# Performance work log

Hardware: AMD Instinct MI355X
Metric: run time of the kernel (lower is better)

Reference implementation:

```python
import jax, jax.numpy as jnp
import numpy as np

Z_DIM = 256
N_MOD = 8
CAT = Z_DIM * N_MOD          # 2048
YS = 1024
B = 4096
EPS = 1e-5


def _layer_norm(x, g, b):
    mu = jnp.mean(x, axis=-1, keepdims=True)
    var = jnp.mean((x - mu) ** 2, axis=-1, keepdims=True)
    return (x - mu) * jax.lax.rsqrt(var + EPS) * g + b


def setup_inputs() -> dict:
    key = jax.random.key(0)
    ks = jax.random.split(key, 16)
    s_cat = 1.0 / np.sqrt(CAT)
    s_ys = 1.0 / np.sqrt(YS)
    return {
        "z_stack": jax.random.normal(ks[0], (N_MOD, B, Z_DIM), jnp.float32),
        "Wq": jax.random.normal(ks[1], (CAT, CAT), jnp.float32) * s_cat,
        "bq": jnp.zeros((CAT,), jnp.float32),
        "Wk": jax.random.normal(ks[2], (CAT, CAT), jnp.float32) * s_cat,
        "bk": jnp.zeros((CAT,), jnp.float32),
        "Wv": jax.random.normal(ks[3], (CAT, CAT), jnp.float32) * s_cat,
        "bv": jnp.zeros((CAT,), jnp.float32),
        "W1": jax.random.normal(ks[4], (CAT, YS), jnp.float32) * s_cat,
        "b1": jnp.zeros((YS,), jnp.float32),
        "W2": jax.random.normal(ks[5], (YS, CAT), jnp.float32) * s_ys,
        "b2": jnp.zeros((CAT,), jnp.float32),
        "ln1_g": jnp.ones((CAT,), jnp.float32),
        "ln1_b": jnp.zeros((CAT,), jnp.float32),
        "ln2_g": jnp.ones((CAT,), jnp.float32),
        "ln2_b": jnp.zeros((CAT,), jnp.float32),
        "Wys": jax.random.normal(ks[6], (CAT, YS), jnp.float32) * s_cat,
        "bys": jnp.zeros((YS,), jnp.float32),
        "Ws": jax.random.normal(ks[7], (N_MOD, YS, Z_DIM), jnp.float32) * s_ys,
        "bs": jnp.zeros((N_MOD, Z_DIM), jnp.float32),
    }


def reference(z_stack, Wq, bq, Wk, bk, Wv, bv, W1, b1, W2, b2,
              ln1_g, ln1_b, ln2_g, ln2_b, Wys, bys, Ws, bs):
    M, Bn, Zd = z_stack.shape
    # torch.cat(z, dim=1): [B, M*Zd]
    x = jnp.transpose(z_stack, (1, 0, 2)).reshape(Bn, M * Zd)
    # self-attention over the batch dim (unscaled, as in source)
    q = x @ Wq + bq
    k = x @ Wk + bk
    v = x @ Wv + bv
    attended = jax.nn.softmax(q @ k.T, axis=-1) @ v  # [B, B] scores
    # dropout is identity in eval mode
    x = _layer_norm(x + attended, ln1_g, ln1_b)
    h = jax.nn.gelu(x @ W1 + b1, approximate=False) @ W2 + b2
    h = _layer_norm(x + h, ln2_g, ln2_b)
    yb = h @ Wys + bys                               # [B, YS]
    # per-module scaling layers, stacked output [M, B, Zd]
    y = jnp.einsum('bs,msz->mbz', yb, Ws) + bs[:, None, :]
    return y
```

## Files before the change

### kernel.cpp

```cpp
#include <hip/hip_runtime.h>
#include <hip/hip_bf16.h>
#include <cstdint>
#include <cstddef>
#include <math.h>

typedef __bf16 bf16x8 __attribute__((ext_vector_type(8)));
typedef float  f32x4  __attribute__((ext_vector_type(4)));

#define DEVI __device__ __forceinline__

static constexpr int BB = 4096;
static constexpr int ZD = 256;

DEVI unsigned short f2bf(float f) {
  __bf16 h = (__bf16)f;
  return __builtin_bit_cast(unsigned short, h);
}
DEVI float bf2f(unsigned short u) {
  return (float)__builtin_bit_cast(__bf16, u);
}

DEVI void gload_lds16(const void* g, void* l) {
  __builtin_amdgcn_global_load_lds(
      (__attribute__((address_space(1))) void*)(g),
      (__attribute__((address_space(3))) void*)(l), 16, 0, 0);
}

DEVI int swz(int L) { return L ^ (((L >> 7) & 7) << 4); }

__global__ __launch_bounds__(256) void pack_x(
    const float* __restrict__ z, unsigned short* __restrict__ x2) {
  const int i = (blockIdx.x * 256 + threadIdx.x) * 4;
  const int m  = i >> 20;
  const int r  = i & 1048575;
  const int b  = r >> 8;
  const int zd = r & 255;
  const float4 v = *(const float4*)(z + i);
  ushort4 h, l;
  h.x = f2bf(v.x); l.x = f2bf(v.x - bf2f(h.x));
  h.y = f2bf(v.y); l.y = f2bf(v.y - bf2f(h.y));
  h.z = f2bf(v.z); l.z = f2bf(v.z - bf2f(h.z));
  h.w = f2bf(v.w); l.w = f2bf(v.w - bf2f(h.w));
  const size_t o2 = (size_t)b * 4096 + m * ZD + zd;
  *(ushort4*)(x2 + o2) = h;
  *(ushort4*)(x2 + o2 + 2048) = l;
}

__global__ __launch_bounds__(256) void transpose_all(
    const float* __restrict__ Wq, const float* __restrict__ Wk,
    const float* __restrict__ Wv, const float* __restrict__ W1,
    const float* __restrict__ W2, const float* __restrict__ Wys,
    const float* __restrict__ Ws,
    unsigned short* __restrict__ Bqk, unsigned short* __restrict__ Wvt,
    unsigned short* __restrict__ W1t, unsigned short* __restrict__ W2t,
    unsigned short* __restrict__ Wyst, unsigned short* __restrict__ Wst) {
  __shared__ float tile[32][33];
  int b = blockIdx.x;
  const float* src;
  unsigned short* dh;
  int C, ldo, nbx, loff = 0;
  if (b < 8192) {
    const int which = b >> 12; b &= 4095;
    src = which ? Wk : Wq;
    dh = Bqk + (size_t)which * 2048 * 4096;
    C = 2048; ldo = 4096; nbx = 64; loff = 2048;
  } else if (b < 12288) { b -= 8192;  src = Wv;  dh = Wvt;  C = 2048; ldo = 2048; nbx = 64; }
  else if (b < 14336)   { b -= 12288; src = W1;  dh = W1t;  C = 1024; ldo = 2048; nbx = 32; }
  else if (b < 16384)   { b -= 14336; src = W2;  dh = W2t;  C = 2048; ldo = 1024; nbx = 64; }
  else if (b < 18432)   { b -= 16384; src = Wys; dh = Wyst; C = 1024; ldo = 2048; nbx = 32; }
  else {
    b -= 18432;
    const int m = b >> 8; b &= 255;
    src = Ws + (size_t)m * 262144;
    dh = Wst + (size_t)m * 262144;
    C = 256; ldo = 1024; nbx = 8;
  }
  const int c0 = (b % nbx) * 32, r0 = (b / nbx) * 32;
  const int tx = threadIdx.x, ty = threadIdx.y;
#pragma unroll
  for (int k = 0; k < 4; ++k)
    tile[ty + 8 * k][tx] = src[(size_t)(r0 + ty + 8 * k) * C + (c0 + tx)];
  __syncthreads();
#pragma unroll
  for (int k = 0; k < 4; ++k) {
    const float f = tile[tx][ty + 8 * k];
    const size_t o = (size_t)(c0 + ty + 8 * k) * ldo + (r0 + tx);
    const unsigned short h = f2bf(f);
    dh[o] = h;
    if (loff) dh[o + loff] = f2bf(f - bf2f(h));
  }
}

#define DOMFMA(QI, QJ, AF, BF)                                            \
  {                                                                       \
    _Pragma("unroll") for (int ks = 0; ks < 2; ++ks) {                    \
      _Pragma("unroll") for (int f = 0; f < 4; ++f) {                     \
        _Pragma("unroll") for (int g = 0; g < 2; ++g) {                   \
          acc[(QI) * 4 + f][(QJ) * 2 + g] =                               \
              __builtin_amdgcn_mfma_f32_16x16x32_bf16(                    \
                  AF[f][ks], BF[g][ks], acc[(QI) * 4 + f][(QJ) * 2 + g],  \
                  0, 0, 0);                                               \
        }                                                                 \
      }                                                                   \
    }                                                                     \
  }

#define PH_SYNC()                                         \
  do {                                                    \
    __builtin_amdgcn_s_barrier();                         \
    asm volatile("s_waitcnt lgkmcnt(0)" ::: "memory");    \
    __builtin_amdgcn_sched_barrier(0);                    \
    __builtin_amdgcn_s_setprio(1);                        \
  } while (0)

#define PH_END()                                          \
  do {                                                    \
    __builtin_amdgcn_s_setprio(0);                        \
    __builtin_amdgcn_sched_barrier(0);                    \
    __builtin_amdgcn_s_barrier();                         \
  } while (0)

template<int EP, bool SEG>
__global__ __launch_bounds__(512, 2) void gemm256(
    const unsigned short* __restrict__ A,
    const unsigned short* __restrict__ Bt,
    const float* __restrict__ bias, const float* __restrict__ bias2,
    float* __restrict__ Cf,
    unsigned short* __restrict__ Ob1, unsigned short* __restrict__ Ob2,
    int Kv, int lda, int ldb, int N, int nbx) {
  extern __shared__ char lds[];
  const int NK = Kv >> 6;
  const int t = threadIdx.x;
  const int lane = t & 63;
  const int w = t >> 6;
  const int wm = w >> 2, wn = w & 3;
  const int lr = lane & 15, kg = lane >> 4;
  int bx, by;
  if (gridDim.x == 256 && nbx == 16) {
    const int xcd = blockIdx.x & 7, i = blockIdx.x >> 3;
    by = (xcd >> 1) * 4 + (i >> 3);
    bx = (xcd & 1) * 8 + (i & 7);
  } else {
    const int q8 = gridDim.x >> 3;
    const int bid = (blockIdx.x & 7) * q8 + (blockIdx.x >> 3);
    bx = bid % nbx; by = bid / nbx;
  }
  const int Ar0 = by * 256, Br0 = bx * 256;

  const int Lb = t << 4;
  const int rowL = Lb >> 7;
  const int colb = swz(Lb) & 127;
  const char* Abase = (const char*)A + (size_t)(Ar0 + rowL) * lda * 2 + colb;
  const char* Bbase = (const char*)Bt + (size_t)(Br0 + rowL) * ldb * 2 + colb;
  const size_t ldaB = (size_t)lda * 128;
  const size_t ldbB = (size_t)ldb * 128;
  char* const ldw = lds + ((t >> 6) << 10);

  auto stageA = [&](int c, int kk, int dst_off) {
    gload_lds16(Abase + (size_t)c * ldaB + ((unsigned)kk << 1), ldw + dst_off);
  };
  auto stageB = [&](int c, int kk, int dst_off) {
    gload_lds16(Bbase + (size_t)c * ldbB + ((unsigned)kk << 1), ldw + dst_off);
  };
  auto rdA = [&](const char* buf, int qi, int f, int ks) {
    const int L = swz(((qi * 64 + f * 16 + lr) << 7) + ks * 64 + kg * 16);
    return *(const bf16x8*)(buf + wm * 16384 + L);
  };
  auto rdB = [&](const char* buf, int qj, int g, int ks) {
    const int L = swz(((wn * 64 + qj * 32 + g * 16 + lr) << 7) + ks * 64 + kg * 16);
    return *(const bf16x8*)(buf + 32768 + L);
  };
  auto kA = [](int k0) { return SEG ? (k0 - ((k0 >> 11) == 2 ? 4096 : 0)) : k0; };
  auto kB = [](int k0) { return SEG ? (k0 - ((k0 >> 11) >= 1 ? 2048 : 0)) : k0; };

  f32x4 acc[8][4] = {};
  bf16x8 af[4][2], b0[2][2], b1[2][2];

  {
    stageA(0, kA(0), 0);
    stageA(1, kA(0), 8192);
    stageA(2, kA(0), 16384);
    stageA(3, kA(0), 24576);
    stageB(0, kB(0), 32768);
    stageB(1, kB(0), 40960);
    stageB(2, kB(0), 49152);
    stageB(3, kB(0), 57344);
    stageA(0, kA(64), 65536 + 0);
    stageA(2, kA(64), 65536 + 16384);
    stageB(0, kB(64), 65536 + 32768);
    stageB(1, kB(64), 65536 + 40960);
    stageB(2, kB(64), 65536 + 49152);
    stageB(3, kB(64), 65536 + 57344);
    asm volatile("s_waitcnt vmcnt(6)" ::: "memory");
    __builtin_amdgcn_sched_barrier(0);
    __builtin_amdgcn_s_barrier();
  }

  for (int tt = 0; tt < NK; ++tt) {
    const int cur = tt & 1;
    const char* buf = lds + cur * 65536;
    const int curo = cur * 65536, nxto = (cur ^ 1) * 65536;
    const int k1 = (tt + 1) * 64, k2 = (tt + 2) * 64;

#pragma unroll
    for (int f = 0; f < 4; ++f)
#pragma unroll
      for (int ks = 0; ks < 2; ++ks) af[f][ks] = rdA(buf, 0, f, ks);
#pragma unroll
    for (int g = 0; g < 2; ++g)
#pragma unroll
      for (int ks = 0; ks < 2; ++ks) b0[g][ks] = rdB(buf, 0, g, ks);
    if (tt + 1 < NK) {
      stageA(1, kA(k1), nxto + 8192);
      stageA(3, kA(k1), nxto + 24576);
    }
    asm volatile("s_waitcnt lgkmcnt(8)" ::: "memory");
    __builtin_amdgcn_sched_barrier(0);
    PH_SYNC();
    DOMFMA(0, 0, af, b0);
    PH_END();

#pragma unroll
    for (int g = 0; g < 2; ++g)
#pragma unroll
      for (int ks = 0; ks < 2; ++ks) b1[g][ks] = rdB(buf, 1, g, ks);
    if (tt + 2 < NK) {
      stageA(0, kA(k2), curo + 0);
      stageA(2, kA(k2), curo + 16384);
    }
    PH_SYNC();
    DOMFMA(0, 1, af, b1);
    PH_END();

#pragma unroll
    for (int f = 0; f < 4; ++f)
#pragma unroll
      for (int ks = 0; ks < 2; ++ks) af[f][ks] = rdA(buf, 1, f, ks);
    if (tt + 2 < NK) {
      stageB(0, kB(k2), curo + 32768);
      stageB(1, kB(k2), curo + 40960);
    }
    PH_SYNC();
    DOMFMA(1, 0, af, b0);
    PH_END();

    if (tt + 2 < NK) {
      stageB(2, kB(k2), curo + 49152);
      stageB(3, kB(k2), curo + 57344);
      asm volatile("s_waitcnt vmcnt(6)" ::: "memory");
    } else {
      asm volatile("s_waitcnt vmcnt(0)" ::: "memory");
    }
    __builtin_amdgcn_sched_barrier(0);
    PH_SYNC();
    DOMFMA(1, 1, af, b1);
    PH_END();
  }

  const int rbase = Ar0 + wm * 128 + kg * 4;
  const int cbase = Br0 + wn * 64 + lr;
#pragma unroll
  for (int rf = 0; rf < 8; ++rf) {
#pragma unroll
    for (int cf = 0; cf < 4; ++cf) {
      const int col = cbase + cf * 16;
#pragma unroll
      for (int q = 0; q < 4; ++q) {
        const int row = rbase + rf * 16 + q;
        float val = acc[rf][cf][q];
        if constexpr (EP == 0) {
          Cf[(size_t)row * N + col] = val;
        } else {
          if (col < 2048) {
            val += bias[col];
            const unsigned short h = f2bf(val);
            Ob1[(size_t)row * 4096 + col] = h;
            Ob1[(size_t)row * 4096 + 2048 + col] = f2bf(val - bf2f(h));
          } else {
            const int c2 = col - 2048;
            val += bias2[c2];
            const unsigned short h = f2bf(val);
            Ob2[(size_t)row * 4096 + c2] = h;
            Ob2[(size_t)row * 4096 + 2048 + c2] = f2bf(val - bf2f(h));
          }
        }
      }
    }
  }
}

template<int EP>
__global__ __launch_bounds__(256) void gemm_bt(
    const unsigned short* __restrict__ Ah,
    const unsigned short* __restrict__ Bh,
    const float* __restrict__ bias,
    float* __restrict__ Cf, unsigned short* __restrict__ Cb,
    int M, int N, int K, int lda, int ldb) {
  __shared__ unsigned short lds[2][128 * 32];
  const int t = threadIdx.x;
  const int lane = t & 63;
  const int w = t >> 6;
  const int wr = (w >> 1) * 64, wc = (w & 1) * 64;
  const int lr = lane & 15, kg = lane >> 4;
  const size_t Ar0 = (size_t)blockIdx.y * 128;
  const size_t Br0 = (size_t)blockIdx.x * 128;

  f32x4 acc[4][4] = {};

  for (int k0 = 0; k0 < K; k0 += 32) {
#pragma unroll
    for (int rnd = 0; rnd < 2; ++rnd) {
      const int e = t * 8 + rnd * 2048;
      const int row = e >> 5, col = e & 31;
      const size_t ga = (Ar0 + row) * (size_t)lda + (k0 + col);
      const size_t gb = (Br0 + row) * (size_t)ldb + (k0 + col);
      const int lo = (w << 9) + rnd * 2048;
      gload_lds16(Ah + ga, &lds[0][lo]);
      gload_lds16(Bh + gb, &lds[1][lo]);
    }
    __syncthreads();
    bf16x8 ah[4], bh[4];
#pragma unroll
    for (int i = 0; i < 4; ++i) {
      ah[i] = *(const bf16x8*)&lds[0][((wr + i * 16 + lr) << 5) + (kg << 3)];
      bh[i] = *(const bf16x8*)&lds[1][((wc + i * 16 + lr) << 5) + (kg << 3)];
    }
#pragma unroll
    for (int i = 0; i < 4; ++i)
#pragma unroll
      for (int j = 0; j < 4; ++j)
        acc[i][j] = __builtin_amdgcn_mfma_f32_16x16x32_bf16(ah[i], bh[j], acc[i][j], 0, 0, 0);
    __syncthreads();
  }

  const int rb = (int)Ar0 + wr + (lane >> 4) * 4;
  const int cb = (int)Br0 + wc + lr;
#pragma unroll
  for (int i = 0; i < 4; ++i) {
#pragma unroll
    for (int j = 0; j < 4; ++j) {
      const int col = cb + j * 16;
      const float bsv = (EP == 5) ? 0.0f : (bias ? bias[col] : 0.0f);
#pragma unroll
      for (int q = 0; q < 4; ++q) {
        const int row = rb + i * 16 + q;
        const float val = acc[i][j][q] + bsv;
        const size_t o = (size_t)row * N + col;
        if constexpr (EP == 0) {
          Cf[o] = val;
        } else if constexpr (EP == 1) {
          Cb[o] = f2bf(val);
        } else if constexpr (EP == 2) {
          const float ge = 0.5f * val * (1.0f + erff(val * 0.70710678118654752f));
          Cb[o] = f2bf(ge);
        } else if constexpr (EP == 4) {
          const size_t oo = (size_t)(col >> 8) * ((size_t)BB * ZD)
                          + (size_t)row * ZD + (col & 255);
          Cf[oo] = val;
        } else {
          Cb[o] = f2bf(val + bias[row]);
        }
      }
    }
  }
}

__global__ __launch_bounds__(256) void softmax_rows(const float* __restrict__ S,
                                                    unsigned short* __restrict__ P) {
  const int row = blockIdx.x;
  const int t = threadIdx.x;
  const int lane = t & 63, w = t >> 6;
  const float* s = S + (size_t)row * 4096;
  float4 v[4];
  float mx = -3.4e38f;
#pragma unroll
  for (int i = 0; i < 4; ++i) {
    v[i] = *(const float4*)(s + (size_t)(t + 256 * i) * 4);
    mx = fmaxf(mx, fmaxf(fmaxf(v[i].x, v[i].y), fmaxf(v[i].z, v[i].w)));
  }
#pragma unroll
  for (int off = 32; off >= 1; off >>= 1) mx = fmaxf(mx, __shfl_xor(mx, off));
  __shared__ float redm[4], redsum[4];
  if (lane == 0) redm[w] = mx;
  __syncthreads();
  mx = fmaxf(fmaxf(redm[0], redm[1]), fmaxf(redm[2], redm[3]));
  float sum = 0.f;
#pragma unroll
  for (int i = 0; i < 4; ++i) {
    v[i].x = expf(v[i].x - mx);
    v[i].y = expf(v[i].y - mx);
    v[i].z = expf(v[i].z - mx);
    v[i].w = expf(v[i].w - mx);
    sum += v[i].x + v[i].y + v[i].z + v[i].w;
  }
#pragma unroll
  for (int off = 32; off >= 1; off >>= 1) sum += __shfl_xor(sum, off);
  if (lane == 0) redsum[w] = sum;
  __syncthreads();
  sum = redsum[0] + redsum[1] + redsum[2] + redsum[3];
  const float inv = 1.0f / sum;
  unsigned short* p = P + (size_t)row * 4096;
#pragma unroll
  for (int i = 0; i < 4; ++i) {
    ushort4 u;
    u.x = f2bf(v[i].x * inv);
    u.y = f2bf(v[i].y * inv);
    u.z = f2bf(v[i].z * inv);
    u.w = f2bf(v[i].w * inv);
    *(ushort4*)(p + (size_t)(t + 256 * i) * 4) = u;
  }
}

template<bool ZG, bool WF32>
__global__ __launch_bounds__(256) void ln_fused(
    const float* __restrict__ a, const float* __restrict__ b,
    const float* __restrict__ g, const float* __restrict__ be,
    float* __restrict__ of, unsigned short* __restrict__ ob) {
  const int row = blockIdx.x;
  const int t = threadIdx.x;
  const int lane = t & 63, w = t >> 6;
  const float* br = b + (size_t)row * 2048;
  float4 x[2];
  float s = 0.f, ss = 0.f;
#pragma unroll
  for (int i = 0; i < 2; ++i) {
    const int o = (t + 256 * i) * 4;
    float4 av;
    if constexpr (ZG) {
      av = *(const float4*)(a + ((size_t)(o >> 8) * 4096 + row) * 256 + (o & 255));
    } else {
      av = *(const float4*)(a + (size_t)row * 2048 + o);
    }
    const float4 bv = *(const float4*)(br + o);
    x[i].x = av.x + bv.x; x[i].y = av.y + bv.y;
    x[i].z = av.z + bv.z; x[i].w = av.w + bv.w;
    s  += x[i].x + x[i].y + x[i].z + x[i].w;
    ss += x[i].x * x[i].x + x[i].y * x[i].y + x[i].z * x[i].z + x[i].w * x[i].w;
  }
#pragma unroll
  for (int off = 32; off >= 1; off >>= 1) {
    s  += __shfl_xor(s, off);
    ss += __shfl_xor(ss, off);
  }
  __shared__ float rs[4], rss[4];
  if (lane == 0) { rs[w] = s; rss[w] = ss; }
  __syncthreads();
  s  = rs[0] + rs[1] + rs[2] + rs[3];
  ss = rss[0] + rss[1] + rss[2] + rss[3];
  const float mu  = s * (1.0f / 2048.0f);
  const float var = ss * (1.0f / 2048.0f) - mu * mu;
  const float inv = rsqrtf(var + 1e-5f);
#pragma unroll
  for (int i = 0; i < 2; ++i) {
    const int o = (t + 256 * i) * 4;
    const float4 gv  = *(const float4*)(g + o);
    const float4 bev = *(const float4*)(be + o);
    float4 y;
    y.x = (x[i].x - mu) * inv * gv.x + bev.x;
    y.y = (x[i].y - mu) * inv * gv.y + bev.y;
    y.z = (x[i].z - mu) * inv * gv.z + bev.z;
    y.w = (x[i].w - mu) * inv * gv.w + bev.w;
    if constexpr (WF32) *(float4*)(of + (size_t)row * 2048 + o) = y;
    ushort4 u;
    u.x = f2bf(y.x); u.y = f2bf(y.y); u.z = f2bf(y.z); u.w = f2bf(y.w);
    *(ushort4*)(ob + (size_t)row * 2048 + o) = u;
  }
}

extern "C" void kernel_launch(void* const* d_in, const int* in_sizes, int n_in,
                              void* d_out, int out_size, void* d_ws, size_t ws_size,
                              hipStream_t stream) {
  (void)in_sizes; (void)n_in; (void)out_size;
  const float* z    = (const float*)d_in[0];
  const float* Wq   = (const float*)d_in[1];
  const float* bq   = (const float*)d_in[2];
  const float* Wk   = (const float*)d_in[3];
  const float* bk   = (const float*)d_in[4];
  const float* Wv   = (const float*)d_in[5];
  const float* bv   = (const float*)d_in[6];
  const float* W1   = (const float*)d_in[7];
  const float* b1   = (const float*)d_in[8];
  const float* W2   = (const float*)d_in[9];
  const float* b2   = (const float*)d_in[10];
  const float* ln1g = (const float*)d_in[11];
  const float* ln1b = (const float*)d_in[12];
  const float* ln2g = (const float*)d_in[13];
  const float* ln2b = (const float*)d_in[14];
  const float* Wys  = (const float*)d_in[15];
  const float* bys  = (const float*)d_in[16];
  const float* Ws   = (const float*)d_in[17];
  const float* bs   = (const float*)d_in[18];
  float* out = (float*)d_out;
  char* ws = (char*)d_ws;

  const size_t MB = 1048576;
  const size_t off_h2   = 0;
  const size_t off_x2   = 32 * MB;
  const size_t off_Bqk  = 64 * MB;
  const size_t off_S    = 32 * MB;
  const size_t off_Aq   = 96 * MB;
  const size_t off_P    = 96 * MB;
  const size_t off_x1f  = 96 * MB;
  const size_t off_Btk  = 128 * MB;
  const size_t off_att  = 128 * MB;
  const size_t off_hmid = 128 * MB;
  const size_t off_ybbf = 136 * MB;
  const size_t off_x1bf = 160 * MB;
  const size_t off_Vt   = 176 * MB;
  const size_t off_x2bf = 176 * MB;
  const size_t off_Wvt  = 192 * MB;
  const size_t off_W1t  = 200 * MB;
  const size_t off_W2t  = 204 * MB;
  const size_t off_Wyst = 208 * MB;
  const size_t off_Wst  = 212 * MB;
  if (ws_size < 216 * MB) return;

#define F32P(o) ((float*)(ws + (o)))
#define BFP(o)  ((unsigned short*)(ws + (o)))

  const int LDSB = 131072;

  pack_x<<<8192, 256, 0, stream>>>(z, BFP(off_x2));
  transpose_all<<<20480, dim3(32, 8), 0, stream>>>(Wq, Wk, Wv, W1, W2, Wys, Ws,
      BFP(off_Bqk), BFP(off_Wvt), BFP(off_W1t), BFP(off_W2t), BFP(off_Wyst), BFP(off_Wst));

  gemm_bt<5><<<dim3(32, 16), 256, 0, stream>>>(BFP(off_Wvt), BFP(off_x2), bv,
      nullptr, BFP(off_Vt), 2048, 4096, 2048, 2048, 4096);

  gemm256<1, true ><<<256, 512, LDSB, stream>>>(BFP(off_x2), BFP(off_Bqk), bq, bk,
      nullptr, BFP(off_Aq), BFP(off_Btk), 6144, 4096, 4096, 4096, 16);

  gemm256<0, true ><<<256, 512, LDSB, stream>>>(BFP(off_Aq), BFP(off_Btk), nullptr, nullptr,
      F32P(off_S), nullptr, nullptr, 6144, 4096, 4096, 4096, 16);

  softmax_rows<<<4096, 256, 0, stream>>>(F32P(off_S), BFP(off_P));
  gemm_bt<0><<<dim3(16, 32), 256, 0, stream>>>(BFP(off_P), BFP(off_Vt), nullptr,
      F32P(off_att), nullptr, 4096, 2048, 4096, 4096, 4096);
  ln_fused<true, true ><<<4096, 256, 0, stream>>>(z, F32P(off_att), ln1g, ln1b,
      F32P(off_x1f), BFP(off_x1bf));

  gemm_bt<2><<<dim3(8, 32), 256, 0, stream>>>(BFP(off_x1bf), BFP(off_W1t), b1,
      nullptr, BFP(off_hmid), 4096, 1024, 2048, 2048, 2048);
  gemm_bt<0><<<dim3(16, 32), 256, 0, stream>>>(BFP(off_hmid), BFP(off_W2t), b2,
      F32P(off_h2), nullptr, 4096, 2048, 1024, 1024, 1024);
  ln_fused<false, false><<<4096, 256, 0, stream>>>(F32P(off_x1f), F32P(off_h2), ln2g, ln2b,
      nullptr, BFP(off_x2bf));

  gemm_bt<1><<<dim3(8, 32), 256, 0, stream>>>(BFP(off_x2bf), BFP(off_Wyst), bys,
      nullptr, BFP(off_ybbf), 4096, 1024, 2048, 2048, 2048);
  gemm_bt<4><<<dim3(16, 32), 256, 0, stream>>>(BFP(off_ybbf), BFP(off_Wst), bs,
      out, nullptr, 4096, 2048, 1024, 1024, 1024);
}
```

Measured before the change: 757.8 us.

## Route P·V through split-K 256-tile GEMM and reduce partials in LayerNorm

The attention P·V product (4096x2048, K=4096) moves from the generic gemm_bt kernel to the larger 256x256-tile gemm256 kernel. It splits K into two slices so 256 blocks fill the device, and each slice writes its own fp32 partial buffer. The first LayerNorm gains an extra input so it adds the second partial while doing the residual add, which folds the split-K reduction into an existing pass. gemm256 also takes its shape parameters as template constants so address arithmetic is resolved at compile time. The cost is an extra 32MB fp32 partial write and read, plus a relocated workspace layout.

```diff
diff --git a/kernel.cpp b/kernel.cpp
--- a/kernel.cpp
+++ b/kernel.cpp
@@ -120,40 +120,47 @@
     __builtin_amdgcn_s_barrier();                         \
   } while (0)
 
-template<int EP, bool SEG>
+template<int EP, bool SEG, int SPLITK, int KV, int LDA, int LDB, int NN, int NBX>
 __global__ __launch_bounds__(512, 2) void gemm256(
     const unsigned short* __restrict__ A,
     const unsigned short* __restrict__ Bt,
     const float* __restrict__ bias, const float* __restrict__ bias2,
     float* __restrict__ Cf,
-    unsigned short* __restrict__ Ob1, unsigned short* __restrict__ Ob2,
-    int Kv, int lda, int ldb, int N, int nbx) {
+    unsigned short* __restrict__ Ob1, unsigned short* __restrict__ Ob2) {
   extern __shared__ char lds[];
-  const int NK = Kv >> 6;
+  constexpr int NK = KV >> 6;
   const int t = threadIdx.x;
   const int lane = t & 63;
   const int w = t >> 6;
   const int wm = w >> 2, wn = w & 3;
   const int lr = lane & 15, kg = lane >> 4;
   int bx, by;
-  if (gridDim.x == 256 && nbx == 16) {
+  if constexpr (SPLITK) {
+    const int bid = (blockIdx.x & 7) * 32 + (blockIdx.x >> 3);
+    const int kslice = bid >> 7;
+    const int tid2 = bid & 127;
+    bx = tid2 & 7; by = tid2 >> 3;
+    A  += kslice * (KV);
+    Bt += kslice * (KV);
+    Cf += (size_t)kslice * ((size_t)4096 * NN);
+  } else if constexpr (NBX == 16) {
     const int xcd = blockIdx.x & 7, i = blockIdx.x >> 3;
     by = (xcd >> 1) * 4 + (i >> 3);
     bx = (xcd & 1) * 8 + (i & 7);
   } else {
     const int q8 = gridDim.x >> 3;
     const int bid = (blockIdx.x & 7) * q8 + (blockIdx.x >> 3);
-    bx = bid % nbx; by = bid / nbx;
+    bx = bid % NBX; by = bid / NBX;
   }
   const int Ar0 = by * 256, Br0 = bx * 256;
 
   const int Lb = t << 4;
   const int rowL = Lb >> 7;
   const int colb = swz(Lb) & 127;
-  const char* Abase = (const char*)A + (size_t)(Ar0 + rowL) * lda * 2 + colb;
-  const char* Bbase = (const char*)Bt + (size_t)(Br0 + rowL) * ldb * 2 + colb;
-  const size_t ldaB = (size_t)lda * 128;
-  const size_t ldbB = (size_t)ldb * 128;
+  const char* Abase = (const char*)A + (size_t)(Ar0 + rowL) * LDA * 2 + colb;
+  const char* Bbase = (const char*)Bt + (size_t)(Br0 + rowL) * LDB * 2 + colb;
+  constexpr size_t ldaB = (size_t)LDA * 128;
+  constexpr size_t ldbB = (size_t)LDB * 128;
   char* const ldw = lds + ((t >> 6) << 10);
 
   auto stageA = [&](int c, int kk, int dst_off) {
@@ -269,7 +276,7 @@
         const int row = rbase + rf * 16 + q;
         float val = acc[rf][cf][q];
         if constexpr (EP == 0) {
-          Cf[(size_t)row * N + col] = val;
+          Cf[(size_t)row * NN + col] = val;
         } else {
           if (col < 2048) {
             val += bias[col];
@@ -414,6 +421,7 @@
 template<bool ZG, bool WF32>
 __global__ __launch_bounds__(256) void ln_fused(
     const float* __restrict__ a, const float* __restrict__ b,
+    const float* __restrict__ c,
     const float* __restrict__ g, const float* __restrict__ be,
     float* __restrict__ of, unsigned short* __restrict__ ob) {
   const int row = blockIdx.x;
@@ -434,6 +442,10 @@
     const float4 bv = *(const float4*)(br + o);
     x[i].x = av.x + bv.x; x[i].y = av.y + bv.y;
     x[i].z = av.z + bv.z; x[i].w = av.w + bv.w;
+    if (c) {
+      const float4 cv = *(const float4*)(c + (size_t)row * 2048 + o);
+      x[i].x += cv.x; x[i].y += cv.y; x[i].z += cv.z; x[i].w += cv.w;
+    }
     s  += x[i].x + x[i].y + x[i].z + x[i].w;
     ss += x[i].x * x[i].x + x[i].y * x[i].y + x[i].z * x[i].z + x[i].w * x[i].w;
   }
@@ -496,13 +508,13 @@
   const size_t MB = 1048576;
   const size_t off_h2   = 0;
   const size_t off_x2   = 32 * MB;
+  const size_t off_S    = 32 * MB;
+  const size_t off_att  = 32 * MB;
   const size_t off_Bqk  = 64 * MB;
-  const size_t off_S    = 32 * MB;
   const size_t off_Aq   = 96 * MB;
   const size_t off_P    = 96 * MB;
   const size_t off_x1f  = 96 * MB;
   const size_t off_Btk  = 128 * MB;
-  const size_t off_att  = 128 * MB;
   const size_t off_hmid = 128 * MB;
   const size_t off_ybbf = 136 * MB;
   const size_t off_x1bf = 160 * MB;
@@ -527,24 +539,24 @@
   gemm_bt<5><<<dim3(32, 16), 256, 0, stream>>>(BFP(off_Wvt), BFP(off_x2), bv,
       nullptr, BFP(off_Vt), 2048, 4096, 2048, 2048, 4096);
 
-  gemm256<1, true ><<<256, 512, LDSB, stream>>>(BFP(off_x2), BFP(off_Bqk), bq, bk,
-      nullptr, BFP(off_Aq), BFP(off_Btk), 6144, 4096, 4096, 4096, 16);
-
-  gemm256<0, true ><<<256, 512, LDSB, stream>>>(BFP(off_Aq), BFP(off_Btk), nullptr, nullptr,
-      F32P(off_S), nullptr, nullptr, 6144, 4096, 4096, 4096, 16);
+  gemm256<1, true, 0, 6144, 4096, 4096, 4096, 16><<<256, 512, LDSB, stream>>>(
+      BFP(off_x2), BFP(off_Bqk), bq, bk, nullptr, BFP(off_Aq), BFP(off_Btk));
+
+  gemm256<0, true, 0, 6144, 4096, 4096, 4096, 16><<<256, 512, LDSB, stream>>>(
+      BFP(off_Aq), BFP(off_Btk), nullptr, nullptr, F32P(off_S), nullptr, nullptr);
 
   softmax_rows<<<4096, 256, 0, stream>>>(F32P(off_S), BFP(off_P));
-  gemm_bt<0><<<dim3(16, 32), 256, 0, stream>>>(BFP(off_P), BFP(off_Vt), nullptr,
-      F32P(off_att), nullptr, 4096, 2048, 4096, 4096, 4096);
-  ln_fused<true, true ><<<4096, 256, 0, stream>>>(z, F32P(off_att), ln1g, ln1b,
-      F32P(off_x1f), BFP(off_x1bf));
+  gemm256<0, false, 1, 2048, 4096, 4096, 2048, 8><<<256, 512, LDSB, stream>>>(
+      BFP(off_P), BFP(off_Vt), nullptr, nullptr, F32P(off_att), nullptr, nullptr);
+  ln_fused<true, true ><<<4096, 256, 0, stream>>>(z, F32P(off_att),
+      F32P(off_att + 32 * MB), ln1g, ln1b, F32P(off_x1f), BFP(off_x1bf));
 
   gemm_bt<2><<<dim3(8, 32), 256, 0, stream>>>(BFP(off_x1bf), BFP(off_W1t), b1,
       nullptr, BFP(off_hmid), 4096, 1024, 2048, 2048, 2048);
   gemm_bt<0><<<dim3(16, 32), 256, 0, stream>>>(BFP(off_hmid), BFP(off_W2t), b2,
       F32P(off_h2), nullptr, 4096, 2048, 1024, 1024, 1024);
-  ln_fused<false, false><<<4096, 256, 0, stream>>>(F32P(off_x1f), F32P(off_h2), ln2g, ln2b,
-      nullptr, BFP(off_x2bf));
+  ln_fused<false, false><<<4096, 256, 0, stream>>>(F32P(off_x1f), F32P(off_h2),
+      nullptr, ln2g, ln2b, nullptr, BFP(off_x2bf));
 
   gemm_bt<1><<<dim3(8, 32), 256, 0, stream>>>(BFP(off_x2bf), BFP(off_Wyst), bys,
       nullptr, BFP(off_ybbf), 4096, 1024, 2048, 2048, 2048);
```

Result: faster. 710.6 us (median of 4 runs) (-6.2%).
